# Kernel optimization log

Measured on AMD Instinct MI355X. Metric: run time of the kernel, lower is better.

The kernel has to match this reference:

```python
import jax, jax.numpy as jnp
import numpy as np

BN_EPS = 1e-5
NN_EPS = 1e-8


def _conv_bn_relu(x, w, gamma, beta, mean, var):
    # x: (B, Cin, N), w: (Cout, Cin) -- 1x1 Conv1d (no bias) + BatchNorm1d (eval) + ReLU
    y = jnp.einsum('oc,bcn->bon', w, x)
    scale = gamma / jnp.sqrt(var + BN_EPS)            # (Cout,)
    shift = beta - mean * scale                       # (Cout,)
    return jax.nn.relu(y * scale[:, None] + shift[:, None])


def setup_inputs() -> dict:
    key = jax.random.key(0)
    ks = jax.random.split(key, 10)
    B, N, M = 4, 2048, 8192
    Cin, Cout = 512, 256
    inp = {
        'x1': jax.random.normal(ks[0], (B, Cin, N), dtype=jnp.float32),
        'p1': jax.random.uniform(ks[1], (B, N, 3), dtype=jnp.float32) * 4.0,
        'x2': jax.random.normal(ks[2], (B, Cout, M), dtype=jnp.float32),
        'p2': jax.random.uniform(ks[3], (B, M, 3), dtype=jnp.float32) * 4.0,
        # up_mlp params
        'w_up': jax.random.normal(ks[4], (Cout, Cin), dtype=jnp.float32) * (1.0 / np.sqrt(Cin)),
        'g_up': jnp.ones((Cout,), jnp.float32),
        'b_up': jnp.zeros((Cout,), jnp.float32),
        'm_up': jax.random.normal(ks[5], (Cout,), dtype=jnp.float32) * 0.1,
        'v_up': jax.random.uniform(ks[6], (Cout,), dtype=jnp.float32) + 0.5,
        # lateral_mlp params
        'w_lat': jax.random.normal(ks[7], (Cout, Cout), dtype=jnp.float32) * (1.0 / np.sqrt(Cout)),
        'g_lat': jnp.ones((Cout,), jnp.float32),
        'b_lat': jnp.zeros((Cout,), jnp.float32),
        'm_lat': jax.random.normal(ks[8], (Cout,), dtype=jnp.float32) * 0.1,
        'v_lat': jax.random.uniform(ks[9], (Cout,), dtype=jnp.float32) + 0.5,
    }
    return inp


def reference(x1, p1, x2, p2, w_up, g_up, b_up, m_up, v_up,
              w_lat, g_lat, b_lat, m_lat, v_lat):
    # up branch: conv1x1 + BN + ReLU on coarse features  (B, Cout, N)
    f1 = _conv_bn_relu(x1, w_up, g_up, b_up, m_up, v_up)

    # three_nn: for each fine point p2 find 3 nearest coarse points p1 (squared dist)
    d2 = (jnp.sum(p2 * p2, -1)[:, :, None]
          + jnp.sum(p1 * p1, -1)[:, None, :]
          - 2.0 * jnp.einsum('bmd,bnd->bmn', p2, p1))        # (B, M, N)
    d2 = jnp.maximum(d2, 0.0)
    neg_d, idx = jax.lax.top_k(-d2, 3)                       # (B, M, 3)
    dist = -neg_d

    # inverse-distance weights
    dist_recip = 1.0 / (dist + NN_EPS)
    weight = dist_recip / jnp.sum(dist_recip, axis=2, keepdims=True)  # (B, M, 3)

    # three_interpolate: gather + weighted sum
    gathered = jax.vmap(lambda f, i: f[:, i])(f1, idx)       # (B, Cout, M, 3)
    interp = jnp.einsum('bcmk,bmk->bcm', gathered, weight)   # (B, Cout, M)

    # lateral branch
    f2 = _conv_bn_relu(x2, w_lat, g_lat, b_lat, m_lat, v_lat)

    return interp + f2, p2
```

## Files before the change

kernel.cpp:

```cpp
#include <hip/hip_runtime.h>
#include <math.h>
#include <float.h>

#define B_    4
#define N_    2048
#define M_    8192
#define CIN_  512
#define COUT_ 256

typedef __attribute__((ext_vector_type(8))) short short8v;
typedef __attribute__((ext_vector_type(4))) float f32x4;

__device__ __forceinline__ void ws_store_f32(float* p, float v) {
    __hip_atomic_store((unsigned int*)p, __float_as_uint(v),
                       __ATOMIC_RELAXED, __HIP_MEMORY_SCOPE_SYSTEM);
}
__device__ __forceinline__ void ws_store_u32(int* p, int v) {
    __hip_atomic_store((unsigned int*)p, (unsigned int)v,
                       __ATOMIC_RELAXED, __HIP_MEMORY_SCOPE_SYSTEM);
}

__global__ __launch_bounds__(64) void inv_kernel() {
    asm volatile("buffer_inv sc0 sc1" ::: "memory");
}

__device__ __forceinline__ unsigned short f2bf(float f) {
    unsigned u = __float_as_uint(f);
    u += 0x7fffu + ((u >> 16) & 1u);
    return (unsigned short)(u >> 16);
}

template<int K, int MODE>
__device__ __forceinline__ void gemm_body(
    char* raw, int b, int c0, int m0,
    const float* __restrict__ X, const float* __restrict__ W,
    const float* __restrict__ gam, const float* __restrict__ bet,
    const float* __restrict__ mu, const float* __restrict__ var,
    float* __restrict__ dst,
    const float* __restrict__ f1t, const float* __restrict__ nnrec, int Mdim)
{
    char* Ab = raw;
    char* Bb = raw + 5120;

    const int tid = threadIdx.x;
    const int l  = tid & 63;
    const int wv = tid >> 6;
    const int wc = wv & 1, wn = wv >> 1;

    f32x4 acc[2][4];
    #pragma unroll
    for (int i = 0; i < 2; ++i)
        #pragma unroll
        for (int j = 0; j < 4; ++j)
            acc[i][j] = (f32x4){0.f, 0.f, 0.f, 0.f};

    const int ksA = tid & 7;
    const int crA = tid >> 3;
    const int kqB = tid >> 5;
    const int mlB = tid & 31;

    float4 ra[4]; float2 rb[4];
    if constexpr (MODE == 1) {
        #pragma unroll
        for (int ni = 0; ni < 4; ++ni) {
            int mg = m0 + wn * 64 + ni * 16 + (l & 15);
            const float* rp = nnrec + ((size_t)b * M_ + mg) * 8;
            ra[ni] = *(const float4*)rp;
            rb[ni] = *(const float2*)(rp + 4);
        }
    }

    float4 wreg[2];
    float  xreg[4][4];
    #pragma unroll
    for (int r = 0; r < 2; ++r)
        wreg[r] = *(const float4*)(W + (size_t)(c0 + crA + 32 * r) * K + ksA * 4);
    #pragma unroll
    for (int jj = 0; jj < 4; ++jj) {
        const float* xp = X + ((size_t)b * K + kqB * 4) * Mdim + m0 + mlB + 32 * jj;
        xreg[jj][0] = xp[0];
        xreg[jj][1] = xp[(size_t)Mdim];
        xreg[jj][2] = xp[(size_t)2 * Mdim];
        xreg[jj][3] = xp[(size_t)3 * Mdim];
    }

    for (int kc = 0; kc < K; kc += 32) {
        #pragma unroll
        for (int r = 0; r < 2; ++r) {
            unsigned lo = f2bf(wreg[r].x) | ((unsigned)f2bf(wreg[r].y) << 16);
            unsigned hi = f2bf(wreg[r].z) | ((unsigned)f2bf(wreg[r].w) << 16);
            *(uint2*)(Ab + (crA + 32 * r) * 80 + ksA * 8) = make_uint2(lo, hi);
        }
        #pragma unroll
        for (int jj = 0; jj < 4; ++jj) {
            unsigned lo = f2bf(xreg[jj][0]) | ((unsigned)f2bf(xreg[jj][1]) << 16);
            unsigned hi = f2bf(xreg[jj][2]) | ((unsigned)f2bf(xreg[jj][3]) << 16);
            *(uint2*)(Bb + (mlB + 32 * jj) * 80 + kqB * 8) = make_uint2(lo, hi);
        }
        if (kc + 32 < K) {
            #pragma unroll
            for (int r = 0; r < 2; ++r)
                wreg[r] = *(const float4*)(W + (size_t)(c0 + crA + 32 * r) * K + (kc + 32) + ksA * 4);
            #pragma unroll
            for (int jj = 0; jj < 4; ++jj) {
                const float* xp = X + ((size_t)b * K + (kc + 32) + kqB * 4) * Mdim + m0 + mlB + 32 * jj;
                xreg[jj][0] = xp[0];
                xreg[jj][1] = xp[(size_t)Mdim];
                xreg[jj][2] = xp[(size_t)2 * Mdim];
                xreg[jj][3] = xp[(size_t)3 * Mdim];
            }
        }
        __syncthreads();
        short8v a[2], bfv[4];
        #pragma unroll
        for (int ci = 0; ci < 2; ++ci)
            a[ci] = *(const short8v*)(Ab + (wc * 32 + ci * 16 + (l & 15)) * 80 + (l >> 4) * 16);
        #pragma unroll
        for (int ni = 0; ni < 4; ++ni)
            bfv[ni] = *(const short8v*)(Bb + (wn * 64 + ni * 16 + (l & 15)) * 80 + (l >> 4) * 16);
        #pragma unroll
        for (int ci = 0; ci < 2; ++ci)
            #pragma unroll
            for (int ni = 0; ni < 4; ++ni)
                acc[ci][ni] = __builtin_amdgcn_mfma_f32_16x16x32_bf16(
                    a[ci], bfv[ni], acc[ci][ni], 0, 0, 0);
        __syncthreads();
    }

    const int lc = (l >> 4) * 4;
    float scA[2][4], shA[2][4];
    #pragma unroll
    for (int ci = 0; ci < 2; ++ci)
        #pragma unroll
        for (int r = 0; r < 4; ++r) {
            int c = c0 + wc * 32 + ci * 16 + lc + r;
            float sc = gam[c] / sqrtf(var[c] + 1e-5f);
            scA[ci][r] = sc;
            shA[ci][r] = bet[c] - mu[c] * sc;
        }

    if constexpr (MODE == 0) {
        float* S = (float*)raw;
        #pragma unroll
        for (int h = 0; h < 2; ++h) {
            if (wn == h) {
                #pragma unroll
                for (int ni = 0; ni < 4; ++ni)
                    #pragma unroll
                    for (int ci = 0; ci < 2; ++ci)
                        #pragma unroll
                        for (int r = 0; r < 4; ++r)
                            S[(ni * 16 + (l & 15)) * 66 + wc * 32 + ci * 16 + lc + r] =
                                fmaxf(acc[ci][ni][r] * scA[ci][r] + shA[ci][r], 0.f);
            }
            __syncthreads();
            #pragma unroll
            for (int i = 0; i < 16; ++i) {
                int e = tid + i * 256;
                int row = e >> 6, c = e & 63;
                ws_store_f32(dst + ((size_t)b * N_ + m0 + h * 64 + row) * COUT_ + c0 + c,
                             S[row * 66 + c]);
            }
            __syncthreads();
        }
    } else {
        #pragma unroll
        for (int ni = 0; ni < 4; ++ni) {
            int mg = m0 + wn * 64 + ni * 16 + (l & 15);
            int   i0 = __float_as_int(ra[ni].x);
            int   i1 = __float_as_int(ra[ni].y);
            int   i2 = __float_as_int(ra[ni].z);
            float w0 = ra[ni].w, w1 = rb[ni].x, w2 = rb[ni].y;
            const float4* g0 = (const float4*)(f1t + ((size_t)b * N_ + i0) * COUT_ + c0 + wc * 32 + lc);
            const float4* g1 = (const float4*)(f1t + ((size_t)b * N_ + i1) * COUT_ + c0 + wc * 32 + lc);
            const float4* g2 = (const float4*)(f1t + ((size_t)b * N_ + i2) * COUT_ + c0 + wc * 32 + lc);
            #pragma unroll
            for (int ci = 0; ci < 2; ++ci) {
                float4 G0 = g0[ci * 4];
                float4 G1 = g1[ci * 4];
                float4 G2 = g2[ci * 4];
                const float* f0 = (const float*)&G0;
                const float* f1 = (const float*)&G1;
                const float* f2 = (const float*)&G2;
                #pragma unroll
                for (int r = 0; r < 4; ++r) {
                    float v = fmaxf(acc[ci][ni][r] * scA[ci][r] + shA[ci][r], 0.f);
                    v = fmaf(w0, f0[r], v);
                    v = fmaf(w1, f1[r], v);
                    v = fmaf(w2, f2[r], v);
                    int c = c0 + wc * 32 + ci * 16 + lc + r;
                    dst[((size_t)b * COUT_ + c) * M_ + mg] = v;
                }
            }
        }
    }
}

__global__ __launch_bounds__(256) void up_kernel(
    const float* __restrict__ x1, const float* __restrict__ w_up,
    const float* __restrict__ g_up, const float* __restrict__ b_up,
    const float* __restrict__ m_up, const float* __restrict__ v_up,
    float* __restrict__ f1t)
{
    __shared__ float4 raw4[1056];
    gemm_body<CIN_, 0>((char*)raw4, blockIdx.z, blockIdx.y * 64, blockIdx.x * 128,
                       x1, w_up, g_up, b_up, m_up, v_up, f1t,
                       nullptr, nullptr, N_);
}

__global__ __launch_bounds__(256) void lat_kernel(
    const float* __restrict__ x2, const float* __restrict__ w_lat,
    const float* __restrict__ g_lat, const float* __restrict__ b_lat,
    const float* __restrict__ m_lat, const float* __restrict__ v_lat,
    const float* __restrict__ f1t, const float* __restrict__ nnrec,
    float* __restrict__ out0)
{
    __shared__ float4 raw4[960];
    gemm_body<COUT_, 1>((char*)raw4, blockIdx.z, blockIdx.y * 64, blockIdx.x * 128,
                        x2, w_lat, g_lat, b_lat, m_lat, v_lat, out0,
                        f1t, nnrec, M_);
}

__device__ __forceinline__ void lex_insert(float e, int j,
    float& D0, float& D1, float& D2, int& I0, int& I1, int& I2)
{
    bool l0 = (e < D0) || (e == D0 && j < I0);
    bool l1 = (e < D1) || (e == D1 && j < I1);
    bool l2 = (e < D2) || (e == D2 && j < I2);
    if (l2) {
        if (l0)      { D2=D1; I2=I1; D1=D0; I1=I0; D0=e; I0=j; }
        else if (l1) { D2=D1; I2=I1; D1=e;  I1=j; }
        else         { D2=e;  I2=j; }
    }
}

__device__ __forceinline__ void bubble_insert(float e, int ie,
    float& D0, float& D1, float& D2, int& I0, int& I1, int& I2)
{
    bool l2 = e < D2;
    D2 = l2 ? e  : D2;
    I2 = l2 ? ie : I2;
    bool s1 = D2 < D1;
    float tf = D1; int ti = I1;
    D1 = s1 ? D2 : D1;  I1 = s1 ? I2 : I1;
    D2 = s1 ? tf : D2;  I2 = s1 ? ti : I2;
    bool s0 = D1 < D0;
    tf = D0; ti = I0;
    D0 = s0 ? D1 : D0;  I0 = s0 ? I1 : I0;
    D1 = s0 ? tf : D1;  I1 = s0 ? ti : I1;
}

__global__ __launch_bounds__(256) void three_nn_kernel(
    const float* __restrict__ p1, const float* __restrict__ p2,
    float* __restrict__ nnrec, float* __restrict__ out1)
{
    __shared__ float4 P[8][257];
    const int b = blockIdx.y;
    #pragma unroll
    for (int r = 0; r < 8; ++r) {
        int n = r * 256 + threadIdx.x;
        float x = p1[((size_t)(b*N_)+n)*3 + 0];
        float y = p1[((size_t)(b*N_)+n)*3 + 1];
        float z = p1[((size_t)(b*N_)+n)*3 + 2];
        float t = x * x;
        t = fmaf(y, y, t);
        t = fmaf(z, z, t);
        P[r][threadIdx.x] = make_float4(x, y, z, t);
    }
    __syncthreads();

    const int m = blockIdx.x * 32 + (threadIdx.x >> 3);
    const int s = threadIdx.x & 7;
    const size_t pbase = ((size_t)(b*M_) + m) * 3;
    const float qx = p2[pbase+0], qy = p2[pbase+1], qz = p2[pbase+2];
    float s2 = qx * qx;
    s2 = fmaf(qy, qy, s2);
    s2 = fmaf(qz, qz, s2);

    float D0a, D1a, D2a, D0b, D1b, D2b, D0c, D1c, D2c, D0d, D1d, D2d;
    int   I0a, I1a, I2a, I0b, I1b, I2b, I0c, I1c, I2c, I0d, I1d, I2d;
    D0a=D1a=D2a=D0b=D1b=D2b=D0c=D1c=D2c=D0d=D1d=D2d=FLT_MAX;
    I0a=I1a=I2a=I0b=I1b=I2b=I0c=I1c=I2c=I0d=I1d=I2d=0x7fffffff;

    const int base = s * 256;
    const float4* Ps = &P[s][0];

    for (int t = 0; t < 256; t += 8) {
        float4 c[8];
        #pragma unroll
        for (int u = 0; u < 8; ++u) c[u] = Ps[t + u];
        float d[8];
        #pragma unroll
        for (int u = 0; u < 8; ++u) {
            float dot = qx * c[u].x;
            dot = fmaf(qy, c[u].y, dot);
            dot = fmaf(qz, c[u].z, dot);
            float d2 = fmaf(-2.0f, dot, s2 + c[u].w);
            d[u] = fmaxf(d2, 0.0f);
        }
        bubble_insert(d[0], base + t + 0, D0a, D1a, D2a, I0a, I1a, I2a);
        bubble_insert(d[1], base + t + 1, D0b, D1b, D2b, I0b, I1b, I2b);
        bubble_insert(d[2], base + t + 2, D0c, D1c, D2c, I0c, I1c, I2c);
        bubble_insert(d[3], base + t + 3, D0d, D1d, D2d, I0d, I1d, I2d);
        bubble_insert(d[4], base + t + 4, D0a, D1a, D2a, I0a, I1a, I2a);
        bubble_insert(d[5], base + t + 5, D0b, D1b, D2b, I0b, I1b, I2b);
        bubble_insert(d[6], base + t + 6, D0c, D1c, D2c, I0c, I1c, I2c);
        bubble_insert(d[7], base + t + 7, D0d, D1d, D2d, I0d, I1d, I2d);
    }

    float D0 = D0a, D1 = D1a, D2 = D2a;
    int   I0 = I0a, I1 = I1a, I2 = I2a;
    lex_insert(D0b, I0b, D0, D1, D2, I0, I1, I2);
    lex_insert(D1b, I1b, D0, D1, D2, I0, I1, I2);
    lex_insert(D2b, I2b, D0, D1, D2, I0, I1, I2);
    lex_insert(D0c, I0c, D0, D1, D2, I0, I1, I2);
    lex_insert(D1c, I1c, D0, D1, D2, I0, I1, I2);
    lex_insert(D2c, I2c, D0, D1, D2, I0, I1, I2);
    lex_insert(D0d, I0d, D0, D1, D2, I0, I1, I2);
    lex_insert(D1d, I1d, D0, D1, D2, I0, I1, I2);
    lex_insert(D2d, I2d, D0, D1, D2, I0, I1, I2);

    #pragma unroll
    for (int st = 1; st <= 4; st <<= 1) {
        float E0 = __shfl_xor(D0, st), E1 = __shfl_xor(D1, st), E2 = __shfl_xor(D2, st);
        int   J0 = __shfl_xor(I0, st), J1 = __shfl_xor(I1, st), J2 = __shfl_xor(I2, st);
        lex_insert(E0, J0, D0, D1, D2, I0, I1, I2);
        lex_insert(E1, J1, D0, D1, D2, I0, I1, I2);
        lex_insert(E2, J2, D0, D1, D2, I0, I1, I2);
    }
    if (s == 0) {
        float r0 = 1.0f / (D0 + 1e-8f);
        float r1 = 1.0f / (D1 + 1e-8f);
        float r2 = 1.0f / (D2 + 1e-8f);
        float sum = (r0 + r1) + r2;
        float* rp = nnrec + ((size_t)(b*M_) + m) * 8;
        ws_store_u32((int*)rp + 0, I0);
        ws_store_u32((int*)rp + 1, I1);
        ws_store_u32((int*)rp + 2, I2);
        ws_store_f32(rp + 3, r0 / sum);
        ws_store_f32(rp + 4, r1 / sum);
        ws_store_f32(rp + 5, r2 / sum);
        size_t o = ((size_t)(b*M_) + m) * 3;
        out1[o+0] = qx; out1[o+1] = qy; out1[o+2] = qz;
    }
}

extern "C" void kernel_launch(void* const* d_in, const int* in_sizes, int n_in,
                              void* d_out, int out_size, void* d_ws, size_t ws_size,
                              hipStream_t stream)
{
    (void)in_sizes; (void)n_in; (void)out_size; (void)ws_size;

    const float* x1    = (const float*)d_in[0];
    const float* p1    = (const float*)d_in[1];
    const float* x2    = (const float*)d_in[2];
    const float* p2    = (const float*)d_in[3];
    const float* w_up  = (const float*)d_in[4];
    const float* g_up  = (const float*)d_in[5];
    const float* b_up  = (const float*)d_in[6];
    const float* m_up  = (const float*)d_in[7];
    const float* v_up  = (const float*)d_in[8];
    const float* w_lat = (const float*)d_in[9];
    const float* g_lat = (const float*)d_in[10];
    const float* b_lat = (const float*)d_in[11];
    const float* m_lat = (const float*)d_in[12];
    const float* v_lat = (const float*)d_in[13];

    float* out0 = (float*)d_out;
    float* out1 = out0 + (size_t)B_ * COUT_ * M_;

    float* f1t   = (float*)d_ws;
    float* nnrec = (float*)((char*)d_ws + (size_t)B_ * N_ * COUT_ * 4);

    up_kernel<<<dim3(N_ / 128, COUT_ / 64, B_), 256, 0, stream>>>(
        x1, w_up, g_up, b_up, m_up, v_up, f1t);

    three_nn_kernel<<<dim3(M_ / 32, B_), 256, 0, stream>>>(
        p1, p2, nnrec, out1);

    inv_kernel<<<dim3(512), 64, 0, stream>>>();

    lat_kernel<<<dim3(M_ / 128, COUT_ / 64, B_), 256, 0, stream>>>(
        x2, w_lat, g_lat, b_lat, m_lat, v_lat, f1t, nnrec, out0);
}
```

Before: 100.4 us.

## Replace brute-force three-NN with per-block uniform grid spatial search

Each three_nn block now sorts the 2048 coarse points into an 8x8x8 uniform grid in shared memory, using an atomic count, a prefix scan and a scatter. Each query then scans its 3x3x3 neighbourhood and expands shell by shell until a coverage bound proves the top three are found. This replaces the exhaustive 2048-point scan per query, and each thread now handles one query instead of eight threads sharing one. In exchange it adds a binning pass in every block and divergent per-query loop lengths. The cell size is chosen for coordinates in [0,4), but clamping and the infinite boundary coverage keep results exact for other inputs.

```diff
diff --git a/kernel.cpp b/kernel.cpp
--- a/kernel.cpp
+++ b/kernel.cpp
@@ -234,115 +234,170 @@
     }
 }
 
-__device__ __forceinline__ void bubble_insert(float e, int ie,
-    float& D0, float& D1, float& D2, int& I0, int& I1, int& I2)
-{
-    bool l2 = e < D2;
-    D2 = l2 ? e  : D2;
-    I2 = l2 ? ie : I2;
-    bool s1 = D2 < D1;
-    float tf = D1; int ti = I1;
-    D1 = s1 ? D2 : D1;  I1 = s1 ? I2 : I1;
-    D2 = s1 ? tf : D2;  I2 = s1 ? ti : I2;
-    bool s0 = D1 < D0;
-    tf = D0; ti = I0;
-    D0 = s0 ? D1 : D0;  I0 = s0 ? I1 : I0;
-    D1 = s0 ? tf : D1;  I1 = s0 ? ti : I1;
-}
+__device__ __forceinline__ float coverage2(float qx, float qy, float qz,
+                                           int cx, int cy, int cz, int r)
+{
+    const float INF = 1e30f;
+    float dxl = (cx - r <= 0) ? INF : qx - (float)(cx - r) * 0.5f;
+    float dxh = (cx + r >= 7) ? INF : (float)(cx + r + 1) * 0.5f - qx;
+    float dyl = (cy - r <= 0) ? INF : qy - (float)(cy - r) * 0.5f;
+    float dyh = (cy + r >= 7) ? INF : (float)(cy + r + 1) * 0.5f - qy;
+    float dzl = (cz - r <= 0) ? INF : qz - (float)(cz - r) * 0.5f;
+    float dzh = (cz + r >= 7) ? INF : (float)(cz + r + 1) * 0.5f - qz;
+    float rc = fminf(fminf(fminf(dxl, dxh), fminf(dyl, dyh)), fminf(dzl, dzh));
+    return rc * rc;
+}
+
+#define NN_EVAL(i)                                                           \
+    {                                                                        \
+        float4 cd = spt[i];                                                  \
+        int   cix = sidx[i];                                                 \
+        float dot = qx * cd.x;                                               \
+        dot = fmaf(qy, cd.y, dot);                                           \
+        dot = fmaf(qz, cd.z, dot);                                           \
+        float d2 = fmaf(-2.0f, dot, s2 + cd.w);                              \
+        d2 = fmaxf(d2, 0.0f);                                                \
+        lex_insert(d2, cix, D0, D1, D2, I0, I1, I2);                         \
+    }
 
 __global__ __launch_bounds__(256) void three_nn_kernel(
     const float* __restrict__ p1, const float* __restrict__ p2,
     float* __restrict__ nnrec, float* __restrict__ out1)
 {
-    __shared__ float4 P[8][257];
+    __shared__ float4 spt[2048];
+    __shared__ int    sidx[2048];
+    __shared__ int    cnt[512];
+    __shared__ int    fill[512];
+    __shared__ int    wsum[4];
+
     const int b = blockIdx.y;
-    #pragma unroll
-    for (int r = 0; r < 8; ++r) {
-        int n = r * 256 + threadIdx.x;
-        float x = p1[((size_t)(b*N_)+n)*3 + 0];
-        float y = p1[((size_t)(b*N_)+n)*3 + 1];
-        float z = p1[((size_t)(b*N_)+n)*3 + 2];
+    const int tid = threadIdx.x;
+
+    cnt[tid] = 0; cnt[tid + 256] = 0;
+    __syncthreads();
+
+    float xr[8], yr[8], zr[8], sr[8];
+    int   cr[8];
+    #pragma unroll
+    for (int u = 0; u < 8; ++u) {
+        int n = u * 256 + tid;
+        float x = p1[((size_t)(b * N_) + n) * 3 + 0];
+        float y = p1[((size_t)(b * N_) + n) * 3 + 1];
+        float z = p1[((size_t)(b * N_) + n) * 3 + 2];
         float t = x * x;
         t = fmaf(y, y, t);
         t = fmaf(z, z, t);
-        P[r][threadIdx.x] = make_float4(x, y, z, t);
-    }
-    __syncthreads();
-
-    const int m = blockIdx.x * 32 + (threadIdx.x >> 3);
-    const int s = threadIdx.x & 7;
-    const size_t pbase = ((size_t)(b*M_) + m) * 3;
-    const float qx = p2[pbase+0], qy = p2[pbase+1], qz = p2[pbase+2];
+        xr[u] = x; yr[u] = y; zr[u] = z; sr[u] = t;
+        int cx = min(max((int)(x * 2.0f), 0), 7);
+        int cy = min(max((int)(y * 2.0f), 0), 7);
+        int cz = min(max((int)(z * 2.0f), 0), 7);
+        int c = (cz * 8 + cy) * 8 + cx;
+        cr[u] = c;
+        atomicAdd(&cnt[c], 1);
+    }
+    __syncthreads();
+
+    int v0 = cnt[2 * tid], v1 = cnt[2 * tid + 1];
+    int tsum = v0 + v1;
+    int sc = tsum;
+    #pragma unroll
+    for (int o = 1; o < 64; o <<= 1) {
+        int nvat = __shfl_up(sc, o);
+        if ((tid & 63) >= o) sc += nvat;
+    }
+    if ((tid & 63) == 63) wsum[tid >> 6] = sc;
+    __syncthreads();
+    int wpre = 0;
+    for (int w = 0; w < (tid >> 6); ++w) wpre += wsum[w];
+    int ex = wpre + sc - tsum;
+    __syncthreads();
+    cnt[2 * tid]     = ex;
+    cnt[2 * tid + 1] = ex + v0;
+    fill[2 * tid]     = ex;
+    fill[2 * tid + 1] = ex + v0;
+    __syncthreads();
+
+    #pragma unroll
+    for (int u = 0; u < 8; ++u) {
+        int pos = atomicAdd(&fill[cr[u]], 1);
+        spt[pos]  = make_float4(xr[u], yr[u], zr[u], sr[u]);
+        sidx[pos] = u * 256 + tid;
+    }
+    __syncthreads();
+
+    const int m = blockIdx.x * 256 + tid;
+    const size_t pbase = ((size_t)(b * M_) + m) * 3;
+    const float qx = p2[pbase + 0], qy = p2[pbase + 1], qz = p2[pbase + 2];
     float s2 = qx * qx;
     s2 = fmaf(qy, qy, s2);
     s2 = fmaf(qz, qz, s2);
 
-    float D0a, D1a, D2a, D0b, D1b, D2b, D0c, D1c, D2c, D0d, D1d, D2d;
-    int   I0a, I1a, I2a, I0b, I1b, I2b, I0c, I1c, I2c, I0d, I1d, I2d;
-    D0a=D1a=D2a=D0b=D1b=D2b=D0c=D1c=D2c=D0d=D1d=D2d=FLT_MAX;
-    I0a=I1a=I2a=I0b=I1b=I2b=I0c=I1c=I2c=I0d=I1d=I2d=0x7fffffff;
-
-    const int base = s * 256;
-    const float4* Ps = &P[s][0];
-
-    for (int t = 0; t < 256; t += 8) {
-        float4 c[8];
-        #pragma unroll
-        for (int u = 0; u < 8; ++u) c[u] = Ps[t + u];
-        float d[8];
-        #pragma unroll
-        for (int u = 0; u < 8; ++u) {
-            float dot = qx * c[u].x;
-            dot = fmaf(qy, c[u].y, dot);
-            dot = fmaf(qz, c[u].z, dot);
-            float d2 = fmaf(-2.0f, dot, s2 + c[u].w);
-            d[u] = fmaxf(d2, 0.0f);
-        }
-        bubble_insert(d[0], base + t + 0, D0a, D1a, D2a, I0a, I1a, I2a);
-        bubble_insert(d[1], base + t + 1, D0b, D1b, D2b, I0b, I1b, I2b);
-        bubble_insert(d[2], base + t + 2, D0c, D1c, D2c, I0c, I1c, I2c);
-        bubble_insert(d[3], base + t + 3, D0d, D1d, D2d, I0d, I1d, I2d);
-        bubble_insert(d[4], base + t + 4, D0a, D1a, D2a, I0a, I1a, I2a);
-        bubble_insert(d[5], base + t + 5, D0b, D1b, D2b, I0b, I1b, I2b);
-        bubble_insert(d[6], base + t + 6, D0c, D1c, D2c, I0c, I1c, I2c);
-        bubble_insert(d[7], base + t + 7, D0d, D1d, D2d, I0d, I1d, I2d);
-    }
-
-    float D0 = D0a, D1 = D1a, D2 = D2a;
-    int   I0 = I0a, I1 = I1a, I2 = I2a;
-    lex_insert(D0b, I0b, D0, D1, D2, I0, I1, I2);
-    lex_insert(D1b, I1b, D0, D1, D2, I0, I1, I2);
-    lex_insert(D2b, I2b, D0, D1, D2, I0, I1, I2);
-    lex_insert(D0c, I0c, D0, D1, D2, I0, I1, I2);
-    lex_insert(D1c, I1c, D0, D1, D2, I0, I1, I2);
-    lex_insert(D2c, I2c, D0, D1, D2, I0, I1, I2);
-    lex_insert(D0d, I0d, D0, D1, D2, I0, I1, I2);
-    lex_insert(D1d, I1d, D0, D1, D2, I0, I1, I2);
-    lex_insert(D2d, I2d, D0, D1, D2, I0, I1, I2);
-
-    #pragma unroll
-    for (int st = 1; st <= 4; st <<= 1) {
-        float E0 = __shfl_xor(D0, st), E1 = __shfl_xor(D1, st), E2 = __shfl_xor(D2, st);
-        int   J0 = __shfl_xor(I0, st), J1 = __shfl_xor(I1, st), J2 = __shfl_xor(I2, st);
-        lex_insert(E0, J0, D0, D1, D2, I0, I1, I2);
-        lex_insert(E1, J1, D0, D1, D2, I0, I1, I2);
-        lex_insert(E2, J2, D0, D1, D2, I0, I1, I2);
-    }
-    if (s == 0) {
-        float r0 = 1.0f / (D0 + 1e-8f);
-        float r1 = 1.0f / (D1 + 1e-8f);
-        float r2 = 1.0f / (D2 + 1e-8f);
-        float sum = (r0 + r1) + r2;
-        float* rp = nnrec + ((size_t)(b*M_) + m) * 8;
-        ws_store_u32((int*)rp + 0, I0);
-        ws_store_u32((int*)rp + 1, I1);
-        ws_store_u32((int*)rp + 2, I2);
-        ws_store_f32(rp + 3, r0 / sum);
-        ws_store_f32(rp + 4, r1 / sum);
-        ws_store_f32(rp + 5, r2 / sum);
-        size_t o = ((size_t)(b*M_) + m) * 3;
-        out1[o+0] = qx; out1[o+1] = qy; out1[o+2] = qz;
-    }
+    const int cxi = min(max((int)(qx * 2.0f), 0), 7);
+    const int cyi = min(max((int)(qy * 2.0f), 0), 7);
+    const int czi = min(max((int)(qz * 2.0f), 0), 7);
+
+    float D0 = FLT_MAX, D1 = FLT_MAX, D2 = FLT_MAX;
+    int   I0 = 0x7fffffff, I1 = 0x7fffffff, I2 = 0x7fffffff;
+
+    {
+        int x0 = max(cxi - 1, 0), x1 = min(cxi + 1, 7);
+        #pragma unroll
+        for (int dz = -1; dz <= 1; ++dz) {
+            int z = czi + dz;
+            if ((unsigned)z > 7u) continue;
+            #pragma unroll
+            for (int dy = -1; dy <= 1; ++dy) {
+                int y = cyi + dy;
+                if ((unsigned)y > 7u) continue;
+                int row = (z * 8 + y) * 8;
+                int st = cnt[row + x0], en = fill[row + x1];
+                for (int i = st; i < en; ++i) NN_EVAL(i)
+            }
+        }
+    }
+
+    float rcov2 = coverage2(qx, qy, qz, cxi, cyi, czi, 1);
+    int r = 2;
+    while (D2 >= rcov2 * 0.999f && r <= 7) {
+        for (int dz = -r; dz <= r; ++dz) {
+            int z = czi + dz;
+            if ((unsigned)z > 7u) continue;
+            for (int dy = -r; dy <= r; ++dy) {
+                int y = cyi + dy;
+                if ((unsigned)y > 7u) continue;
+                int row = (z * 8 + y) * 8;
+                bool edge = (dz == r) || (dz == -r) || (dy == r) || (dy == -r);
+                if (edge) {
+                    int x0 = max(cxi - r, 0), x1 = min(cxi + r, 7);
+                    int st = cnt[row + x0], en = fill[row + x1];
+                    for (int i = st; i < en; ++i) NN_EVAL(i)
+                } else {
+                    for (int sgn = -1; sgn <= 1; sgn += 2) {
+                        int x = cxi + sgn * r;
+                        if ((unsigned)x > 7u) continue;
+                        int st = cnt[row + x], en = fill[row + x];
+                        for (int i = st; i < en; ++i) NN_EVAL(i)
+                    }
+                }
+            }
+        }
+        rcov2 = coverage2(qx, qy, qz, cxi, cyi, czi, r);
+        ++r;
+    }
+
+    float r0 = 1.0f / (D0 + 1e-8f);
+    float r1 = 1.0f / (D1 + 1e-8f);
+    float r2 = 1.0f / (D2 + 1e-8f);
+    float sum = (r0 + r1) + r2;
+    float* rp = nnrec + ((size_t)(b * M_) + m) * 8;
+    ws_store_u32((int*)rp + 0, I0);
+    ws_store_u32((int*)rp + 1, I1);
+    ws_store_u32((int*)rp + 2, I2);
+    ws_store_f32(rp + 3, r0 / sum);
+    ws_store_f32(rp + 4, r1 / sum);
+    ws_store_f32(rp + 5, r2 / sum);
+    size_t o = ((size_t)(b * M_) + m) * 3;
+    out1[o + 0] = qx; out1[o + 1] = qy; out1[o + 2] = qz;
 }
 
 extern "C" void kernel_launch(void* const* d_in, const int* in_sizes, int n_in,
@@ -375,7 +430,7 @@
     up_kernel<<<dim3(N_ / 128, COUT_ / 64, B_), 256, 0, stream>>>(
         x1, w_up, g_up, b_up, m_up, v_up, f1t);
 
-    three_nn_kernel<<<dim3(M_ / 32, B_), 256, 0, stream>>>(
+    three_nn_kernel<<<dim3(M_ / 256, B_), 256, 0, stream>>>(
         p1, p2, nnrec, out1);
 
     inv_kernel<<<dim3(512), 64, 0, stream>>>();
```

New measurement: 216.4 us. 2.16x slower.
